# Optimization experiments

Hardware: AMD Instinct MI355X
Metric: run time of the kernel (lower is better)

Reference implementation:

```python
import jax, jax.numpy as jnp
import numpy as np

EPS = 1e-6


def _build_cayley():
    # Blade ordering of the CEGNN CliffordAlgebra for Cl(3,0): combinations order
    # 1, e1, e2, e3, e12, e13, e23, e123. Metric (1,1,1) => e_k^2 = +1.
    blades = [(), (0,), (1,), (2,), (0, 1), (0, 2), (1, 2), (0, 1, 2)]
    index = {b: i for i, b in enumerate(blades)}
    cayley = np.zeros((8, 8, 8), dtype=np.float32)
    for i, a in enumerate(blades):
        for j, b in enumerate(blades):
            arr = list(a) + list(b)
            sign = 1
            # bubble sort, counting transpositions of anticommuting generators
            for p in range(len(arr)):
                for q in range(len(arr) - 1):
                    if arr[q] > arr[q + 1]:
                        arr[q], arr[q + 1] = arr[q + 1], arr[q]
                        sign = -sign
            # contract equal adjacent generators (e_k e_k = +1)
            out = []
            q = 0
            while q < len(arr):
                if q + 1 < len(arr) and arr[q] == arr[q + 1]:
                    q += 2
                else:
                    out.append(arr[q])
                    q += 1
            cayley[i, j, index[tuple(out)]] = sign
    return cayley


_CAYLEY = jnp.asarray(_build_cayley())  # (8, 8, 8)


def _mvlinear(x, W, b):
    # MVLinear(subspaces=False): channel mixing shared across blades,
    # bias embedded into the scalar (grade-0) blade only.
    y = jnp.einsum("bmi,nm->bni", x, W)
    return y.at[:, :, 0].add(b)


def setup_inputs() -> dict:
    key = jax.random.key(0)
    ks = jax.random.split(key, 7)
    B, Cin, Ch, Cout = 16384, 512, 512, 512
    s = 1.0 / np.sqrt(Cin)
    return {
        "vec1": jax.random.normal(ks[0], (B, Cin, 8), dtype=jnp.float32),
        "W_left": jax.random.normal(ks[1], (Ch, Cin), dtype=jnp.float32) * s,
        "b_left": jax.random.normal(ks[2], (Ch,), dtype=jnp.float32) * 0.01,
        "W_right": jax.random.normal(ks[3], (Ch, Cin), dtype=jnp.float32) * s,
        "b_right": jax.random.normal(ks[4], (Ch,), dtype=jnp.float32) * 0.01,
        "W_out": jax.random.normal(ks[5], (Cout, Ch), dtype=jnp.float32) * s,
        "b_out": jax.random.normal(ks[6], (Cout,), dtype=jnp.float32) * 0.01,
        "a_norm": jnp.ones((Cout,), dtype=jnp.float32),
    }


def reference(vec1, W_left, b_left, W_right, b_right, W_out, b_out, a_norm):
    vec_right = _mvlinear(vec1, W_right, b_right)   # (B, Ch, 8)
    vec_left = _mvlinear(vec1, W_left, b_left)      # (B, Ch, 8)
    # geometric product via the sparse Cayley table of Cl(3,0)
    gp = jnp.einsum("bmi,ijk,bmj->bmk", vec_left, _CAYLEY, vec_right)
    out = _mvlinear(gp, W_out, b_out)               # (B, Cout, 8)
    # MVLayerNorm: per-multivector quadratic-form norm (all-positive metric =>
    # sqrt of sum of squared blade coefficients), averaged over channels.
    norm = jnp.sqrt(jnp.sum(out * out, axis=-1, keepdims=True))  # (B, Cout, 1)
    norm = jnp.mean(norm, axis=1, keepdims=True) + EPS           # (B, 1, 1)
    return a_norm[None, :, None] * out / norm
```

## Files before the change

kernel.cpp:

```cpp
#include <hip/hip_runtime.h>
#include <cstdint>
#include <cstddef>

typedef _Float16 f16;
typedef __attribute__((ext_vector_type(8))) _Float16 f16x8;
typedef __attribute__((ext_vector_type(4))) _Float16 f16x4;
typedef __attribute__((ext_vector_type(4))) float f32x4;

#define MFMA_F16(a, b, c) __builtin_amdgcn_mfma_f32_16x16x32_f16((a), (b), (c), 0, 0, 0)

#define GL2LDS(gsrc, ldst)                                                  \
    __builtin_amdgcn_global_load_lds(                                        \
        (const __attribute__((address_space(1))) void*)(gsrc),               \
        (__attribute__((address_space(3))) void*)(ldst), 16, 0, 0)

#define WAITV(n) asm volatile("s_waitcnt vmcnt(" #n ")" ::: "memory")
#define BAR() __builtin_amdgcn_s_barrier()

#define SWZ(row) (((row) >> 1) & 3)


__global__ __launch_bounds__(256) void k0(const float* __restrict__ x,
                                          const float* __restrict__ wl,
                                          const float* __restrict__ wr,
                                          const float* __restrict__ wo,
                                          f16* __restrict__ wdst,
                                          f16* __restrict__ xt) {
    const int bid = blockIdx.x;
    if (bid >= 8192) {
        int i = (bid - 8192) * 256 + threadIdx.x;
        wdst[i]          = (f16)wl[i];
        wdst[262144 + i] = (f16)wr[i];
        wdst[524288 + i] = (f16)wo[i];
        return;
    }
    const int b = (bid >> 1) * 4 + (threadIdx.x >> 6);
    const int m = (bid & 1) * 256 + (threadIdx.x & 63) * 4;
    const float* src = x + ((size_t)b * 512 + m) * 8;
    f32x4 v[8];
#pragma unroll
    for (int u = 0; u < 8; ++u) v[u] = *(const f32x4*)(src + u * 4);
#pragma unroll
    for (int i = 0; i < 8; ++i) {
        f16x4 w;
#pragma unroll
        for (int j = 0; j < 4; ++j) w[j] = (f16)v[j * 2 + (i >> 2)][i & 3];
        *(f16x4*)(xt + (size_t)i * 8388608 + (size_t)b * 512 + m) = w;
    }
}

__global__ __launch_bounds__(1024, 4) void k1(
    const f16* __restrict__ xt, const f16* __restrict__ wf,
    const float* __restrict__ bl_p, const float* __restrict__ br_p,
    char* gp_out)
{
    __shared__ __align__(16) f16 AsF[3 * 8192];
    __shared__ __align__(16) f16 WsF[3 * 8192];

    const int L = blockIdx.x;
    const int xcd = L & 7, sl = L >> 3;
    const int bt = xcd * 64 + (sl >> 2), ct = sl & 3;
    const int b0 = bt * 32, n0 = ct * 128;

    const int tid = threadIdx.x, lane = tid & 63, wv = tid >> 6;
    const int wb = wv >> 3, wn = wv & 7;
    const int r_lo = lane & 15, s_hi = lane >> 4;

    const int ab = tid >> 7, arw = (tid >> 2) & 31, ac = (tid & 3) ^ SWZ(arw);
    const f16* aS = xt + (size_t)ab * 8388608 + (size_t)(b0 + arw) * 512 + ac * 8;
    const int wsd = tid >> 9, wnr = (tid >> 2) & 127, wc = (tid & 3) ^ SWZ(wnr);
    const f16* wS = wf + (size_t)wsd * 262144 + (size_t)(n0 + wnr) * 512 + wc * 8;

    f16* aD = AsF + wv * 512;
    f16* wD = WsF + wv * 512;

    const int ar = wb * 16 + r_lo;
    const int aoff = ar * 32 + ((s_hi ^ SWZ(ar)) << 3);
    const int nloc = wn * 16 + r_lo;
    const int boff = nloc * 32 + ((s_hi ^ SWZ(nloc)) << 3);

    f32x4 accL[8], accR[8];
    const f32x4 zero = {0.f, 0.f, 0.f, 0.f};
#pragma unroll
    for (int i = 0; i < 8; ++i) { accL[i] = zero; accR[i] = zero; }

    auto stage = [&](int kt, int buf) {
        GL2LDS(aS + kt * 32, aD + buf * 8192);
        GL2LDS(wS + kt * 32, wD + buf * 8192);
    };

    stage(0, 0);
    stage(1, 1);

#pragma unroll
    for (int kk = 0; kk < 16; ++kk) {
        if (kk + 2 < 16) stage(kk + 2, (kk + 2) % 3);
        if (kk <= 13)      { WAITV(4); }
        else if (kk == 14) { WAITV(2); }
        else               { WAITV(0); }
        BAR();
        const f16* Ab = AsF + (kk % 3) * 8192;
        const f16* Wb = WsF + (kk % 3) * 8192;
        f16x8 bL = *(const f16x8*)(Wb + boff);
        f16x8 bR = *(const f16x8*)(Wb + 4096 + boff);
#pragma unroll
        for (int i = 0; i < 8; ++i) {
            f16x8 a = *(const f16x8*)(Ab + i * 1024 + aoff);
            accL[i] = MFMA_F16(a, bL, accL[i]);
            accR[i] = MFMA_F16(a, bR, accR[i]);
        }
        BAR();
    }

    const int n_g = n0 + nloc;
    const float blv = bl_p[n_g], brv = br_p[n_g];
#pragma unroll
    for (int rr = 0; rr < 4; ++rr) {
        const int b_g = b0 + wb * 16 + s_hi * 4 + rr;
        float Lv[8], Rv[8];
#pragma unroll
        for (int i = 0; i < 8; ++i) { Lv[i] = accL[i][rr]; Rv[i] = accR[i][rr]; }
        Lv[0] += blv; Rv[0] += brv;
        float g[8];
        g[0] = Lv[0]*Rv[0]+Lv[1]*Rv[1]+Lv[2]*Rv[2]+Lv[3]*Rv[3]-Lv[4]*Rv[4]-Lv[5]*Rv[5]-Lv[6]*Rv[6]-Lv[7]*Rv[7];
        g[1] = Lv[0]*Rv[1]+Lv[1]*Rv[0]-Lv[2]*Rv[4]-Lv[3]*Rv[5]+Lv[4]*Rv[2]+Lv[5]*Rv[3]-Lv[6]*Rv[7]-Lv[7]*Rv[6];
        g[2] = Lv[0]*Rv[2]+Lv[1]*Rv[4]+Lv[2]*Rv[0]-Lv[3]*Rv[6]-Lv[4]*Rv[1]+Lv[5]*Rv[7]+Lv[6]*Rv[3]+Lv[7]*Rv[5];
        g[3] = Lv[0]*Rv[3]+Lv[1]*Rv[5]+Lv[2]*Rv[6]+Lv[3]*Rv[0]-Lv[4]*Rv[7]-Lv[5]*Rv[1]-Lv[6]*Rv[2]-Lv[7]*Rv[4];
        g[4] = Lv[0]*Rv[4]+Lv[1]*Rv[2]-Lv[2]*Rv[1]+Lv[3]*Rv[7]+Lv[4]*Rv[0]-Lv[5]*Rv[6]+Lv[6]*Rv[5]+Lv[7]*Rv[3];
        g[5] = Lv[0]*Rv[5]+Lv[1]*Rv[3]-Lv[2]*Rv[7]-Lv[3]*Rv[1]+Lv[4]*Rv[6]+Lv[5]*Rv[0]-Lv[6]*Rv[4]-Lv[7]*Rv[2];
        g[6] = Lv[0]*Rv[6]+Lv[1]*Rv[7]+Lv[2]*Rv[3]-Lv[3]*Rv[2]-Lv[4]*Rv[5]+Lv[5]*Rv[4]+Lv[6]*Rv[0]+Lv[7]*Rv[1];
        g[7] = Lv[0]*Rv[7]+Lv[1]*Rv[6]-Lv[2]*Rv[5]+Lv[3]*Rv[4]+Lv[4]*Rv[3]-Lv[5]*Rv[2]+Lv[6]*Rv[1]+Lv[7]*Rv[0];
        char* dst = gp_out + (size_t)b_g * 16384 + (size_t)n_g * 2;
#pragma unroll
        for (int i = 0; i < 8; ++i) *(f16*)(dst + (size_t)i * 1024) = (f16)g[i];
    }
}

__global__ __launch_bounds__(1024, 4) void k2(
    const char* gp_in, const f16* __restrict__ wo,
    const float* __restrict__ bo_p, const float* __restrict__ an_p,
    float* outp)
{
    __shared__ __align__(16) f16 AsF[3 * 4096];
    __shared__ __align__(16) f16 BsF[3 * 16384];
    __shared__ float red[16][16];

    const int b0 = blockIdx.x * 16;
    const int tid = threadIdx.x, lane = tid & 63, wv = tid >> 6;
    const int r_lo = lane & 15, s_hi = lane >> 4;

    const int abl = tid >> 6, arw = (tid >> 2) & 15, agp = (tid & 3) ^ SWZ(arw);
    const char* aS = gp_in + (size_t)(b0 + arw) * 16384 + (size_t)(abl & 7) * 1024 + agp * 16;
    const int bn = tid >> 2, bg = (tid & 3) ^ SWZ(bn);
    const f16* bS0 = wo + (size_t)bn * 512 + bg * 8;
    const f16* bS1 = wo + (size_t)(bn + 256) * 512 + bg * 8;

    f16* aD  = AsF + wv * 512;
    f16* bD0 = BsF + wv * 512;
    f16* bD1 = BsF + 8192 + wv * 512;

    const int aoff = r_lo * 32 + ((s_hi ^ SWZ(r_lo)) << 3);
    const int nl0 = wv * 32 + r_lo, nl1 = nl0 + 16;
    const int boff0 = nl0 * 32 + ((s_hi ^ SWZ(nl0)) << 3);
    const int boff1 = nl1 * 32 + ((s_hi ^ SWZ(nl1)) << 3);

    f32x4 acc[2][8];
    const f32x4 zero = {0.f, 0.f, 0.f, 0.f};
#pragma unroll
    for (int st = 0; st < 2; ++st)
#pragma unroll
        for (int i = 0; i < 8; ++i) acc[st][i] = zero;

    auto stage = [&](int kt, int buf) {
        if (wv < 8) GL2LDS(aS + kt * 64, aD + buf * 4096);
        GL2LDS(bS0 + kt * 32, bD0 + buf * 16384);
        GL2LDS(bS1 + kt * 32, bD1 + buf * 16384);
    };

    stage(0, 0);
    stage(1, 1);

#pragma unroll
    for (int kk = 0; kk < 16; ++kk) {
        if (kk + 2 < 16) stage(kk + 2, (kk + 2) % 3);
        if (kk <= 13)      { if (wv < 8) { WAITV(6); } else { WAITV(4); } }
        else if (kk == 14) { if (wv < 8) { WAITV(3); } else { WAITV(2); } }
        else               { WAITV(0); }
        BAR();
        const f16* Ab = AsF + (kk % 3) * 4096;
        const f16* Bb = BsF + (kk % 3) * 16384;
        f16x8 bf0 = *(const f16x8*)(Bb + boff0);
        f16x8 bf1 = *(const f16x8*)(Bb + boff1);
#pragma unroll
        for (int i = 0; i < 8; ++i) {
            f16x8 a = *(const f16x8*)(Ab + i * 512 + aoff);
            acc[0][i] = MFMA_F16(a, bf0, acc[0][i]);
            acc[1][i] = MFMA_F16(a, bf1, acc[1][i]);
        }
        BAR();
    }

    const float bo0 = bo_p[nl0], bo1 = bo_p[nl1];
    const float an0 = an_p[nl0], an1 = an_p[nl1];

    float partial[4];
#pragma unroll
    for (int rr = 0; rr < 4; ++rr) {
        float o = acc[0][0][rr] + bo0;
        float ss = o * o;
#pragma unroll
        for (int i = 1; i < 8; ++i) ss += acc[0][i][rr] * acc[0][i][rr];
        float s = sqrtf(ss);
        o = acc[1][0][rr] + bo1;
        ss = o * o;
#pragma unroll
        for (int i = 1; i < 8; ++i) ss += acc[1][i][rr] * acc[1][i][rr];
        partial[rr] = s + sqrtf(ss);
    }
#pragma unroll
    for (int off = 1; off < 16; off <<= 1)
#pragma unroll
        for (int rr = 0; rr < 4; ++rr) partial[rr] += __shfl_xor(partial[rr], off);
    if (r_lo == 0)
#pragma unroll
        for (int rr = 0; rr < 4; ++rr) red[s_hi * 4 + rr][wv] = partial[rr];
    __syncthreads();

#pragma unroll
    for (int rr = 0; rr < 4; ++rr) {
        float tot = 0.f;
#pragma unroll
        for (int w = 0; w < 16; ++w) tot += red[s_hi * 4 + rr][w];
        const float inv = 1.0f / (tot * (1.0f / 512.0f) + 1e-6f);
        const float sc0 = an0 * inv, sc1 = an1 * inv;
        const int b_g = b0 + s_hi * 4 + rr;
        float* dst = outp + (size_t)b_g * 4096;
        f32x4 v;
        v[0] = (acc[0][0][rr] + bo0) * sc0;
        v[1] = acc[0][1][rr] * sc0; v[2] = acc[0][2][rr] * sc0; v[3] = acc[0][3][rr] * sc0;
        *(f32x4*)(dst + (size_t)nl0 * 8) = v;
        v[0] = acc[0][4][rr] * sc0; v[1] = acc[0][5][rr] * sc0;
        v[2] = acc[0][6][rr] * sc0; v[3] = acc[0][7][rr] * sc0;
        *(f32x4*)(dst + (size_t)nl0 * 8 + 4) = v;
        v[0] = (acc[1][0][rr] + bo1) * sc1;
        v[1] = acc[1][1][rr] * sc1; v[2] = acc[1][2][rr] * sc1; v[3] = acc[1][3][rr] * sc1;
        *(f32x4*)(dst + (size_t)nl1 * 8) = v;
        v[0] = acc[1][4][rr] * sc1; v[1] = acc[1][5][rr] * sc1;
        v[2] = acc[1][6][rr] * sc1; v[3] = acc[1][7][rr] * sc1;
        *(f32x4*)(dst + (size_t)nl1 * 8 + 4) = v;
    }
}

extern "C" void kernel_launch(void* const* d_in, const int* in_sizes, int n_in,
                              void* d_out, int out_size, void* d_ws, size_t ws_size,
                              hipStream_t stream) {
    const float* x  = (const float*)d_in[0];
    const float* wl = (const float*)d_in[1];
    const float* bl = (const float*)d_in[2];
    const float* wr = (const float*)d_in[3];
    const float* br = (const float*)d_in[4];
    const float* wo = (const float*)d_in[5];
    const float* bo = (const float*)d_in[6];
    const float* an = (const float*)d_in[7];
    f16* wf = (f16*)d_ws;
    f16* xt = wf + (1 << 20);

    hipLaunchKernelGGL(k0, dim3(9216), dim3(256), 0, stream, x, wl, wr, wo, wf, xt);
    hipLaunchKernelGGL(k1, dim3(2048), dim3(1024), 0, stream, xt, wf, bl, br, (char*)d_out);
    hipLaunchKernelGGL(k2, dim3(1024), dim3(1024), 0, stream,
                       (const char*)d_out, wf + 524288, bo, an, (float*)d_out);
}
```

Baseline: 445.8 us.

## Load weight fragments directly into registers instead of staging through LDS

In both GEMM kernels the weight tile is no longer copied into shared memory. Each lane now loads its own B fragment straight from global memory into double-buffered registers, one k-step ahead, while only the activation tile stays in the triple-buffered LDS pipeline. MFMA groups are also wrapped in s_setprio to raise wave priority during compute. This cuts LDS traffic and footprint, which may allow more resident blocks, but it adds uncached-pattern global loads per wave and relies on L2 to absorb the duplicate weight reads across blocks.

```diff
diff --git a/kernel.cpp b/kernel.cpp
--- a/kernel.cpp
+++ b/kernel.cpp
@@ -16,6 +16,7 @@
 
 #define WAITV(n) asm volatile("s_waitcnt vmcnt(" #n ")" ::: "memory")
 #define BAR() __builtin_amdgcn_s_barrier()
+#define PRIO(n) __builtin_amdgcn_s_setprio(n)
 
 #define SWZ(row) (((row) >> 1) & 3)
 
@@ -55,7 +56,6 @@
     char* gp_out)
 {
     __shared__ __align__(16) f16 AsF[3 * 8192];
-    __shared__ __align__(16) f16 WsF[3 * 8192];
 
     const int L = blockIdx.x;
     const int xcd = L & 7, sl = L >> 3;
@@ -68,58 +68,76 @@
 
     const int ab = tid >> 7, arw = (tid >> 2) & 31, ac = (tid & 3) ^ SWZ(arw);
     const f16* aS = xt + (size_t)ab * 8388608 + (size_t)(b0 + arw) * 512 + ac * 8;
-    const int wsd = tid >> 9, wnr = (tid >> 2) & 127, wc = (tid & 3) ^ SWZ(wnr);
-    const f16* wS = wf + (size_t)wsd * 262144 + (size_t)(n0 + wnr) * 512 + wc * 8;
-
     f16* aD = AsF + wv * 512;
-    f16* wD = WsF + wv * 512;
 
     const int ar = wb * 16 + r_lo;
-    const int aoff = ar * 32 + ((s_hi ^ SWZ(ar)) << 3);
-    const int nloc = wn * 16 + r_lo;
-    const int boff = nloc * 32 + ((s_hi ^ SWZ(nloc)) << 3);
-
-    f32x4 accL[8], accR[8];
+    const int arow = ar * 32 + ((s_hi ^ SWZ(ar)) << 3);
+
+    const int chrow = n0 + wn * 16 + r_lo;
+    const f16* bPL = wf + (size_t)chrow * 512 + s_hi * 8;
+    const f16* bPR = bPL + 262144;
+
+    f32x4 acc[8][2];
     const f32x4 zero = {0.f, 0.f, 0.f, 0.f};
 #pragma unroll
-    for (int i = 0; i < 8; ++i) { accL[i] = zero; accR[i] = zero; }
-
-    auto stage = [&](int kt, int buf) {
-        GL2LDS(aS + kt * 32, aD + buf * 8192);
-        GL2LDS(wS + kt * 32, wD + buf * 8192);
-    };
-
-    stage(0, 0);
-    stage(1, 1);
-
-#pragma unroll
-    for (int kk = 0; kk < 16; ++kk) {
-        if (kk + 2 < 16) stage(kk + 2, (kk + 2) % 3);
-        if (kk <= 13)      { WAITV(4); }
-        else if (kk == 14) { WAITV(2); }
+    for (int i = 0; i < 8; ++i) { acc[i][0] = zero; acc[i][1] = zero; }
+
+    auto stageA = [&](int kt, int buf) { GL2LDS(aS + kt * 32, aD + buf * 8192); };
+
+    f16x8 bregs[2][2];
+    stageA(0, 0);
+    bregs[0][0] = *(const f16x8*)bPL;
+    bregs[0][1] = *(const f16x8*)bPR;
+    stageA(1, 1);
+
+#pragma unroll
+    for (int kt = 0; kt < 16; ++kt) {
+        if (kt + 2 < 16) stageA(kt + 2, (kt + 2) % 3);
+        if (kt < 15) {
+            bregs[(kt + 1) & 1][0] = *(const f16x8*)(bPL + (kt + 1) * 32);
+            bregs[(kt + 1) & 1][1] = *(const f16x8*)(bPR + (kt + 1) * 32);
+        }
+        if (kt <= 13)      { WAITV(3); }
+        else if (kt == 14) { WAITV(2); }
         else               { WAITV(0); }
         BAR();
-        const f16* Ab = AsF + (kk % 3) * 8192;
-        const f16* Wb = WsF + (kk % 3) * 8192;
-        f16x8 bL = *(const f16x8*)(Wb + boff);
-        f16x8 bR = *(const f16x8*)(Wb + 4096 + boff);
-#pragma unroll
-        for (int i = 0; i < 8; ++i) {
-            f16x8 a = *(const f16x8*)(Ab + i * 1024 + aoff);
-            accL[i] = MFMA_F16(a, bL, accL[i]);
-            accR[i] = MFMA_F16(a, bR, accR[i]);
+        const f16* Ab = AsF + (kt % 3) * 8192;
+        const f16x8 bL = bregs[kt & 1][0];
+        const f16x8 bR = bregs[kt & 1][1];
+        {
+            f16x8 a0 = *(const f16x8*)(Ab + 0 * 1024 + arow);
+            f16x8 a1 = *(const f16x8*)(Ab + 1 * 1024 + arow);
+            f16x8 a2 = *(const f16x8*)(Ab + 2 * 1024 + arow);
+            f16x8 a3 = *(const f16x8*)(Ab + 3 * 1024 + arow);
+            PRIO(1);
+            acc[0][0] = MFMA_F16(a0, bL, acc[0][0]); acc[0][1] = MFMA_F16(a0, bR, acc[0][1]);
+            acc[1][0] = MFMA_F16(a1, bL, acc[1][0]); acc[1][1] = MFMA_F16(a1, bR, acc[1][1]);
+            acc[2][0] = MFMA_F16(a2, bL, acc[2][0]); acc[2][1] = MFMA_F16(a2, bR, acc[2][1]);
+            acc[3][0] = MFMA_F16(a3, bL, acc[3][0]); acc[3][1] = MFMA_F16(a3, bR, acc[3][1]);
+            PRIO(0);
+        }
+        {
+            f16x8 a4 = *(const f16x8*)(Ab + 4 * 1024 + arow);
+            f16x8 a5 = *(const f16x8*)(Ab + 5 * 1024 + arow);
+            f16x8 a6 = *(const f16x8*)(Ab + 6 * 1024 + arow);
+            f16x8 a7 = *(const f16x8*)(Ab + 7 * 1024 + arow);
+            PRIO(1);
+            acc[4][0] = MFMA_F16(a4, bL, acc[4][0]); acc[4][1] = MFMA_F16(a4, bR, acc[4][1]);
+            acc[5][0] = MFMA_F16(a5, bL, acc[5][0]); acc[5][1] = MFMA_F16(a5, bR, acc[5][1]);
+            acc[6][0] = MFMA_F16(a6, bL, acc[6][0]); acc[6][1] = MFMA_F16(a6, bR, acc[6][1]);
+            acc[7][0] = MFMA_F16(a7, bL, acc[7][0]); acc[7][1] = MFMA_F16(a7, bR, acc[7][1]);
+            PRIO(0);
         }
         BAR();
     }
 
-    const int n_g = n0 + nloc;
-    const float blv = bl_p[n_g], brv = br_p[n_g];
+    const float blv = bl_p[chrow], brv = br_p[chrow];
 #pragma unroll
     for (int rr = 0; rr < 4; ++rr) {
         const int b_g = b0 + wb * 16 + s_hi * 4 + rr;
         float Lv[8], Rv[8];
 #pragma unroll
-        for (int i = 0; i < 8; ++i) { Lv[i] = accL[i][rr]; Rv[i] = accR[i][rr]; }
+        for (int i = 0; i < 8; ++i) { Lv[i] = acc[i][0][rr]; Rv[i] = acc[i][1][rr]; }
         Lv[0] += blv; Rv[0] += brv;
         float g[8];
         g[0] = Lv[0]*Rv[0]+Lv[1]*Rv[1]+Lv[2]*Rv[2]+Lv[3]*Rv[3]-Lv[4]*Rv[4]-Lv[5]*Rv[5]-Lv[6]*Rv[6]-Lv[7]*Rv[7];
@@ -130,7 +148,7 @@
         g[5] = Lv[0]*Rv[5]+Lv[1]*Rv[3]-Lv[2]*Rv[7]-Lv[3]*Rv[1]+Lv[4]*Rv[6]+Lv[5]*Rv[0]-Lv[6]*Rv[4]-Lv[7]*Rv[2];
         g[6] = Lv[0]*Rv[6]+Lv[1]*Rv[7]+Lv[2]*Rv[3]-Lv[3]*Rv[2]-Lv[4]*Rv[5]+Lv[5]*Rv[4]+Lv[6]*Rv[0]+Lv[7]*Rv[1];
         g[7] = Lv[0]*Rv[7]+Lv[1]*Rv[6]-Lv[2]*Rv[5]+Lv[3]*Rv[4]+Lv[4]*Rv[3]-Lv[5]*Rv[2]+Lv[6]*Rv[1]+Lv[7]*Rv[0];
-        char* dst = gp_out + (size_t)b_g * 16384 + (size_t)n_g * 2;
+        char* dst = gp_out + (size_t)b_g * 16384 + (size_t)chrow * 2;
 #pragma unroll
         for (int i = 0; i < 8; ++i) *(f16*)(dst + (size_t)i * 1024) = (f16)g[i];
     }
@@ -142,7 +160,6 @@
     float* outp)
 {
     __shared__ __align__(16) f16 AsF[3 * 4096];
-    __shared__ __align__(16) f16 BsF[3 * 16384];
     __shared__ float red[16][16];
 
     const int b0 = blockIdx.x * 16;
@@ -151,51 +168,66 @@
 
     const int abl = tid >> 6, arw = (tid >> 2) & 15, agp = (tid & 3) ^ SWZ(arw);
     const char* aS = gp_in + (size_t)(b0 + arw) * 16384 + (size_t)(abl & 7) * 1024 + agp * 16;
-    const int bn = tid >> 2, bg = (tid & 3) ^ SWZ(bn);
-    const f16* bS0 = wo + (size_t)bn * 512 + bg * 8;
-    const f16* bS1 = wo + (size_t)(bn + 256) * 512 + bg * 8;
-
-    f16* aD  = AsF + wv * 512;
-    f16* bD0 = BsF + wv * 512;
-    f16* bD1 = BsF + 8192 + wv * 512;
+    f16* aD = AsF + wv * 512;
 
     const int aoff = r_lo * 32 + ((s_hi ^ SWZ(r_lo)) << 3);
+
     const int nl0 = wv * 32 + r_lo, nl1 = nl0 + 16;
-    const int boff0 = nl0 * 32 + ((s_hi ^ SWZ(nl0)) << 3);
-    const int boff1 = nl1 * 32 + ((s_hi ^ SWZ(nl1)) << 3);
-
-    f32x4 acc[2][8];
+    const f16* bQ0 = wo + (size_t)nl0 * 512 + s_hi * 8;
+    const f16* bQ1 = wo + (size_t)nl1 * 512 + s_hi * 8;
+
+    f32x4 acc[8][2];
     const f32x4 zero = {0.f, 0.f, 0.f, 0.f};
 #pragma unroll
-    for (int st = 0; st < 2; ++st)
-#pragma unroll
-        for (int i = 0; i < 8; ++i) acc[st][i] = zero;
-
-    auto stage = [&](int kt, int buf) {
-        if (wv < 8) GL2LDS(aS + kt * 64, aD + buf * 4096);
-        GL2LDS(bS0 + kt * 32, bD0 + buf * 16384);
-        GL2LDS(bS1 + kt * 32, bD1 + buf * 16384);
+    for (int i = 0; i < 8; ++i) { acc[i][0] = zero; acc[i][1] = zero; }
+
+    auto stageA = [&](int kt, int buf) {
+        if (tid < 512) GL2LDS(aS + (size_t)kt * 64, aD + buf * 4096);
     };
 
-    stage(0, 0);
-    stage(1, 1);
-
-#pragma unroll
-    for (int kk = 0; kk < 16; ++kk) {
-        if (kk + 2 < 16) stage(kk + 2, (kk + 2) % 3);
-        if (kk <= 13)      { if (wv < 8) { WAITV(6); } else { WAITV(4); } }
-        else if (kk == 14) { if (wv < 8) { WAITV(3); } else { WAITV(2); } }
+    f16x8 bregs[2][2];
+    stageA(0, 0);
+    bregs[0][0] = *(const f16x8*)bQ0;
+    bregs[0][1] = *(const f16x8*)bQ1;
+    stageA(1, 1);
+
+#pragma unroll
+    for (int kt = 0; kt < 16; ++kt) {
+        if (kt + 2 < 16) stageA(kt + 2, (kt + 2) % 3);
+        if (kt < 15) {
+            bregs[(kt + 1) & 1][0] = *(const f16x8*)(bQ0 + (kt + 1) * 32);
+            bregs[(kt + 1) & 1][1] = *(const f16x8*)(bQ1 + (kt + 1) * 32);
+        }
+        if (kt <= 13)      { if (wv < 8) { WAITV(3); } else { WAITV(2); } }
+        else if (kt == 14) { WAITV(2); }
         else               { WAITV(0); }
         BAR();
-        const f16* Ab = AsF + (kk % 3) * 4096;
-        const f16* Bb = BsF + (kk % 3) * 16384;
-        f16x8 bf0 = *(const f16x8*)(Bb + boff0);
-        f16x8 bf1 = *(const f16x8*)(Bb + boff1);
-#pragma unroll
-        for (int i = 0; i < 8; ++i) {
-            f16x8 a = *(const f16x8*)(Ab + i * 512 + aoff);
-            acc[0][i] = MFMA_F16(a, bf0, acc[0][i]);
-            acc[1][i] = MFMA_F16(a, bf1, acc[1][i]);
+        const f16* Ab = AsF + (kt % 3) * 4096;
+        const f16x8 b0f = bregs[kt & 1][0];
+        const f16x8 b1f = bregs[kt & 1][1];
+        {
+            f16x8 a0 = *(const f16x8*)(Ab + 0 * 512 + aoff);
+            f16x8 a1 = *(const f16x8*)(Ab + 1 * 512 + aoff);
+            f16x8 a2 = *(const f16x8*)(Ab + 2 * 512 + aoff);
+            f16x8 a3 = *(const f16x8*)(Ab + 3 * 512 + aoff);
+            PRIO(1);
+            acc[0][0] = MFMA_F16(a0, b0f, acc[0][0]); acc[0][1] = MFMA_F16(a0, b1f, acc[0][1]);
+            acc[1][0] = MFMA_F16(a1, b0f, acc[1][0]); acc[1][1] = MFMA_F16(a1, b1f, acc[1][1]);
+            acc[2][0] = MFMA_F16(a2, b0f, acc[2][0]); acc[2][1] = MFMA_F16(a2, b1f, acc[2][1]);
+            acc[3][0] = MFMA_F16(a3, b0f, acc[3][0]); acc[3][1] = MFMA_F16(a3, b1f, acc[3][1]);
+            PRIO(0);
+        }
+        {
+            f16x8 a4 = *(const f16x8*)(Ab + 4 * 512 + aoff);
+            f16x8 a5 = *(const f16x8*)(Ab + 5 * 512 + aoff);
+            f16x8 a6 = *(const f16x8*)(Ab + 6 * 512 + aoff);
+            f16x8 a7 = *(const f16x8*)(Ab + 7 * 512 + aoff);
+            PRIO(1);
+            acc[4][0] = MFMA_F16(a4, b0f, acc[4][0]); acc[4][1] = MFMA_F16(a4, b1f, acc[4][1]);
+            acc[5][0] = MFMA_F16(a5, b0f, acc[5][0]); acc[5][1] = MFMA_F16(a5, b1f, acc[5][1]);
+            acc[6][0] = MFMA_F16(a6, b0f, acc[6][0]); acc[6][1] = MFMA_F16(a6, b1f, acc[6][1]);
+            acc[7][0] = MFMA_F16(a7, b0f, acc[7][0]); acc[7][1] = MFMA_F16(a7, b1f, acc[7][1]);
+            PRIO(0);
         }
         BAR();
     }
@@ -209,12 +241,12 @@
         float o = acc[0][0][rr] + bo0;
         float ss = o * o;
 #pragma unroll
-        for (int i = 1; i < 8; ++i) ss += acc[0][i][rr] * acc[0][i][rr];
+        for (int i = 1; i < 8; ++i) ss += acc[i][0][rr] * acc[i][0][rr];
         float s = sqrtf(ss);
-        o = acc[1][0][rr] + bo1;
+        o = acc[0][1][rr] + bo1;
         ss = o * o;
 #pragma unroll
-        for (int i = 1; i < 8; ++i) ss += acc[1][i][rr] * acc[1][i][rr];
+        for (int i = 1; i < 8; ++i) ss += acc[i][1][rr] * acc[i][1][rr];
         partial[rr] = s + sqrtf(ss);
     }
 #pragma unroll
@@ -237,16 +269,16 @@
         float* dst = outp + (size_t)b_g * 4096;
         f32x4 v;
         v[0] = (acc[0][0][rr] + bo0) * sc0;
-        v[1] = acc[0][1][rr] * sc0; v[2] = acc[0][2][rr] * sc0; v[3] = acc[0][3][rr] * sc0;
+        v[1] = acc[1][0][rr] * sc0; v[2] = acc[2][0][rr] * sc0; v[3] = acc[3][0][rr] * sc0;
         *(f32x4*)(dst + (size_t)nl0 * 8) = v;
-        v[0] = acc[0][4][rr] * sc0; v[1] = acc[0][5][rr] * sc0;
-        v[2] = acc[0][6][rr] * sc0; v[3] = acc[0][7][rr] * sc0;
+        v[0] = acc[4][0][rr] * sc0; v[1] = acc[5][0][rr] * sc0;
+        v[2] = acc[6][0][rr] * sc0; v[3] = acc[7][0][rr] * sc0;
         *(f32x4*)(dst + (size_t)nl0 * 8 + 4) = v;
-        v[0] = (acc[1][0][rr] + bo1) * sc1;
-        v[1] = acc[1][1][rr] * sc1; v[2] = acc[1][2][rr] * sc1; v[3] = acc[1][3][rr] * sc1;
+        v[0] = (acc[0][1][rr] + bo1) * sc1;
+        v[1] = acc[1][1][rr] * sc1; v[2] = acc[2][1][rr] * sc1; v[3] = acc[3][1][rr] * sc1;
         *(f32x4*)(dst + (size_t)nl1 * 8) = v;
-        v[0] = acc[1][4][rr] * sc1; v[1] = acc[1][5][rr] * sc1;
-        v[2] = acc[1][6][rr] * sc1; v[3] = acc[1][7][rr] * sc1;
+        v[0] = acc[4][1][rr] * sc1; v[1] = acc[5][1][rr] * sc1;
+        v[2] = acc[6][1][rr] * sc1; v[3] = acc[7][1][rr] * sc1;
         *(f32x4*)(dst + (size_t)nl1 * 8 + 4) = v;
     }
 }
```

Result: slower. 528.3 us (+18.5%).
